# Performance work log

Hardware: AMD Instinct MI355X
Metric: run time of the kernel (lower is better)

Reference implementation:

```python
import jax, jax.numpy as jnp
import numpy as np

B, S, D, H = 2, 2048, 2048, 16
HD = D // H          # head dim 128
R = 64               # qk_rope_head_dim
LR = 64              # kv_low_rank_dim
FF = 2048            # ffn_dim per expert
E = 8                # num routed experts
K = 2                # top_k
ROPE_BASE = 10000.0
LN_EPS = 1e-5


def setup_inputs() -> dict:
    key = jax.random.key(0)
    ks = jax.random.split(key, 20)
    def rn(k, shape, fan_in):
        return jax.random.normal(k, shape, jnp.float32) * (1.0 / np.sqrt(fan_in))
    return {
        "hidden_states": jax.random.normal(ks[0], (B, S, D), jnp.float32),
        "position_ids": jnp.arange(S, dtype=jnp.int32)[None, :],
        # attention projections, stored [in, out]
        "Wq": rn(ks[1], (D, D), D), "Wk": rn(ks[2], (D, D), D), "Wv": rn(ks[3], (D, D), D),
        "Wkc": rn(ks[4], (HD, LR), HD), "Wvc": rn(ks[5], (HD, LR), HD),
        "Wqa": rn(ks[6], (HD, LR), HD), "Wqg": rn(ks[7], (HD, HD), HD),
        "Wov": rn(ks[8], (LR, HD), LR), "Wo": rn(ks[9], (D, D), D),
        "ln1_w": jnp.ones((D,), jnp.float32), "ln1_b": jnp.zeros((D,), jnp.float32),
        "ln2_w": jnp.ones((D,), jnp.float32), "ln2_b": jnp.zeros((D,), jnp.float32),
        # MoE
        "Wg": rn(ks[10], (D, E), D),
        "We1": rn(ks[11], (E, D, FF), D), "We2": rn(ks[12], (E, FF, D), FF), "We3": rn(ks[13], (E, D, FF), D),
        "Ws1": rn(ks[14], (D, FF), D), "Ws2": rn(ks[15], (FF, D), FF), "Ws3": rn(ks[16], (D, FF), D),
    }


def _layernorm(x, w, b):
    mu = jnp.mean(x, -1, keepdims=True)
    var = jnp.mean(jnp.square(x - mu), -1, keepdims=True)
    return (x - mu) * jax.lax.rsqrt(var + LN_EPS) * w + b


def _rotate_half(x):
    h = x.shape[-1] // 2
    return jnp.concatenate([-x[..., h:], x[..., :h]], axis=-1)


def _rope_cos_sin(position_ids, dtype):
    inv_freq = 1.0 / (ROPE_BASE ** (jnp.arange(0, R, 2, dtype=jnp.float32) / R))
    t = jnp.arange(S, dtype=jnp.float32)
    freqs = t[:, None] * inv_freq[None, :]           # [S, R/2]
    emb = jnp.concatenate([freqs, freqs], -1)        # [S, R]
    cos = jnp.cos(emb).astype(dtype)[position_ids][:, :, None, :]  # [1,S,1,R]
    sin = jnp.sin(emb).astype(dtype)[position_ids][:, :, None, :]
    return cos, sin


def reference(hidden_states, position_ids, Wq, Wk, Wv, Wkc, Wvc, Wqa, Wqg, Wov, Wo,
              ln1_w, ln1_b, ln2_w, ln2_b, Wg, We1, We2, We3, Ws1, Ws2, Ws3):
    x = _layernorm(hidden_states, ln1_w, ln1_b)
    # ---- MLA attention ----
    q = (x @ Wq).reshape(B, S, H, HD)
    k = (x @ Wk).reshape(B, S, H, HD)
    v = (x @ Wv).reshape(B, S, H, HD)
    cos, sin = _rope_cos_sin(position_ids, x.dtype)
    qr = q[..., :R] * cos + _rotate_half(q[..., :R]) * sin
    kr = k[..., :R] * cos + _rotate_half(k[..., :R]) * sin
    q = jnp.concatenate([qr, q[..., R:]], -1)
    k = jnp.concatenate([kr, k[..., R:]], -1)
    k_c = k @ Wkc                                   # [B,S,H,LR]
    v_c = v @ Wvc                                   # [B,S,H,LR]
    q_a = q @ Wqa                                   # [B,S,H,LR]
    q_gate = q @ Wqg                                # [B,S,H,HD]
    scores = jnp.einsum('bqhr,bkhr->bhqk', q_a, k_c) / np.sqrt(LR)
    attw = jax.nn.softmax(scores.astype(jnp.float32), axis=-1).astype(q.dtype)
    att_c = jnp.einsum('bhqk,bkhr->bqhr', attw, v_c)  # [B,S,H,LR]
    uplift = att_c @ Wov                              # [B,S,H,HD]
    gated = (jax.nn.silu(q_gate) * uplift).reshape(B, S, D)
    attn_out = gated @ Wo
    h = hidden_states + attn_out
    # ---- MoE with shared expert ----
    xf = _layernorm(h, ln2_w, ln2_b).reshape(-1, D)   # [T, D]
    shared = (jax.nn.silu(xf @ Ws1) * (xf @ Ws3)) @ Ws2
    logits = xf @ Wg                                  # [T, E]
    probs = jax.nn.softmax(logits.astype(jnp.float32), axis=-1)
    topw, topi = jax.lax.top_k(probs, K)
    topw = topw / jnp.sum(topw, -1, keepdims=True)
    T = xf.shape[0]
    combine = jnp.zeros((T, E), xf.dtype).at[jnp.arange(T)[:, None], topi].set(topw.astype(xf.dtype))
    h1 = jnp.einsum('td,edf->etf', xf, We1)
    h3 = jnp.einsum('td,edf->etf', xf, We3)
    eout = jnp.einsum('etf,efd->etd', jax.nn.silu(h1) * h3, We2)
    moe = shared + jnp.einsum('te,etd->td', combine, eout)
    return h + moe.reshape(B, S, D)
```

## Files before the change

### kernel.cpp

```cpp
#include <hip/hip_runtime.h>
#include <math.h>

typedef __bf16 bf16;
typedef __bf16 bf16x8 __attribute__((ext_vector_type(8)));
typedef float f32x4 __attribute__((ext_vector_type(4)));

#define B_ 2
#define S_ 2048
#define D_ 2048
#define H_ 16
#define FF_ 2048
#define E_ 8
#define T_ 4096
#define TH_ 65536
#define CAP_ 4096

#define MFMA_(a, b, c) __builtin_amdgcn_mfma_f32_16x16x32_bf16(a, b, c, 0, 0, 0)

__device__ __forceinline__ int swz(int row, int byteoff) {
  return row * 128 + (byteoff ^ ((row & 7) << 4));
}
__device__ __forceinline__ int swzf(int row, int byteoff) {
  return row * 256 + (byteoff ^ ((row & 7) << 5));
}

__device__ __forceinline__ void split2(float x, bf16& h, bf16& m) {
  h = (bf16)x;
  m = (bf16)(x - (float)h);
}

__device__ __forceinline__ void frag_split(const char* p, int off, bf16x8& r0, bf16x8& r1) {
  f32x4 u = *(const f32x4*)(p + off);
  f32x4 v = *(const f32x4*)(p + off + 16);
#pragma unroll
  for (int j = 0; j < 4; j++) { bf16 a, b; split2(u[j], a, b); r0[j] = a; r1[j] = b; }
#pragma unroll
  for (int j = 0; j < 4; j++) { bf16 a, b; split2(v[j], a, b); r0[4 + j] = a; r1[4 + j] = b; }
}

__device__ __forceinline__ f32x4 dot3(bf16x8 a0, bf16x8 a1,
                                      bf16x8 b0, bf16x8 b1, f32x4 c) {
  c = MFMA_(a0, b0, c);
  c = MFMA_(a0, b1, c);
  c = MFMA_(a1, b0, c);
  return c;
}

__device__ __forceinline__ float blk_sum(float v, float* sbuf, int tid) {
#pragma unroll
  for (int mk = 32; mk; mk >>= 1) v += __shfl_xor(v, mk);
  __syncthreads();
  if ((tid & 63) == 0) sbuf[tid >> 6] = v;
  __syncthreads();
  return sbuf[0] + sbuf[1] + sbuf[2] + sbuf[3];
}

__global__ __launch_bounds__(256) void k_transpose32(const float* __restrict__ src,
                                                     float* __restrict__ dst, int R, int C) {
  __shared__ float tile[32][33];
  int tx = threadIdx.x, ty = threadIdx.y;
  int c0 = blockIdx.x * 32, r0 = blockIdx.y * 32;
#pragma unroll
  for (int j = 0; j < 32; j += 8) tile[ty + j][tx] = src[(size_t)(r0 + ty + j) * C + (c0 + tx)];
  __syncthreads();
#pragma unroll
  for (int j = 0; j < 32; j += 8)
    dst[(size_t)(c0 + ty + j) * R + (r0 + tx)] = tile[tx][ty + j];
}

__global__ __launch_bounds__(256) void k_transpose32b3(const float* __restrict__ s0,
                                                       const float* __restrict__ s1x,
                                                       const float* __restrict__ s2,
                                                       float* __restrict__ dbase) {
  __shared__ float tile[32][33];
  int z = blockIdx.z;
  const float* src = z == 0 ? s0 : (z == 1 ? s1x : s2);
  float* dst = dbase + (size_t)z * 8192;
  int tx = threadIdx.x, ty = threadIdx.y;
  int c0 = blockIdx.x * 32, r0 = blockIdx.y * 32;
#pragma unroll
  for (int j = 0; j < 32; j += 8) tile[ty + j][tx] = src[(size_t)(r0 + ty + j) * 64 + (c0 + tx)];
  __syncthreads();
#pragma unroll
  for (int j = 0; j < 32; j += 8)
    dst[(size_t)(c0 + ty + j) * 128 + (r0 + tx)] = tile[tx][ty + j];
}

__global__ __launch_bounds__(256) void k_transpose_sh3(const float* __restrict__ s0,
                                                       const float* __restrict__ s1x,
                                                       const float* __restrict__ s2,
                                                       bf16* __restrict__ dbase) {
  __shared__ float tile[32][33];
  int z = blockIdx.z;
  const float* src = z == 0 ? s0 : (z == 1 ? s1x : s2);
  bf16* dst = dbase + (size_t)z * 4194304;
  int tx = threadIdx.x, ty = threadIdx.y;
  int c0 = blockIdx.x * 32, r0 = blockIdx.y * 32;
#pragma unroll
  for (int j = 0; j < 32; j += 8) tile[ty + j][tx] = src[(size_t)(r0 + ty + j) * 2048 + (c0 + tx)];
  __syncthreads();
#pragma unroll
  for (int j = 0; j < 32; j += 8)
    dst[(size_t)(c0 + ty + j) * 2048 + (r0 + tx)] = (bf16)tile[tx][ty + j];
}

template <int MODE>
__global__ __launch_bounds__(256) void k_transpose_moe(const float* __restrict__ W1,
                                                       const float* __restrict__ W3,
                                                       bf16* __restrict__ dstB, int eBase) {
  __shared__ float tile[32][33];
  int tx = threadIdx.x, ty = threadIdx.y;
  int z = blockIdx.z;
  const float* src;
  if (MODE == 0) src = ((z & 1) ? W3 : W1) + (size_t)(eBase + (z >> 1)) * 4194304;
  else src = W1 + (size_t)(eBase + z) * 4194304;
  bf16* dst = dstB + (size_t)z * 4194304;
  int c0 = blockIdx.x * 32, r0 = blockIdx.y * 32;
#pragma unroll
  for (int j = 0; j < 32; j += 8) tile[ty + j][tx] = src[(size_t)(r0 + ty + j) * 2048 + (c0 + tx)];
  __syncthreads();
#pragma unroll
  for (int j = 0; j < 32; j += 8)
    dst[(size_t)(c0 + ty + j) * 2048 + (r0 + tx)] = (bf16)tile[tx][ty + j];
}

__global__ __launch_bounds__(256) void k_transpose_split(const float* __restrict__ src,
                                                         bf16* __restrict__ dh, bf16* __restrict__ dl,
                                                         int R, int C) {
  __shared__ float tile[32][33];
  int tx = threadIdx.x, ty = threadIdx.y;
  int c0 = blockIdx.x * 32, r0 = blockIdx.y * 32;
#pragma unroll
  for (int j = 0; j < 32; j += 8) tile[ty + j][tx] = src[(size_t)(r0 + ty + j) * C + (c0 + tx)];
  __syncthreads();
#pragma unroll
  for (int j = 0; j < 32; j += 8) {
    float v = tile[tx][ty + j];
    bf16 h, l;
    split2(v, h, l);
    size_t o = (size_t)(c0 + ty + j) * R + (r0 + tx);
    dh[o] = h;
    dl[o] = l;
  }
}

__global__ __launch_bounds__(256) void k_transpose_split3(const float* __restrict__ s0,
                                                          const float* __restrict__ s1x,
                                                          const float* __restrict__ s2,
                                                          bf16* __restrict__ dbase) {
  __shared__ float tile[32][33];
  int z = blockIdx.z;
  const float* src = z == 0 ? s0 : (z == 1 ? s1x : s2);
  bf16* dh = dbase + (size_t)z * 8388608;
  bf16* dl = dh + 4194304;
  int tx = threadIdx.x, ty = threadIdx.y;
  int c0 = blockIdx.x * 32, r0 = blockIdx.y * 32;
#pragma unroll
  for (int j = 0; j < 32; j += 8) tile[ty + j][tx] = src[(size_t)(r0 + ty + j) * 2048 + (c0 + tx)];
  __syncthreads();
#pragma unroll
  for (int j = 0; j < 32; j += 8) {
    float v = tile[tx][ty + j];
    bf16 h, l;
    split2(v, h, l);
    size_t o = (size_t)(c0 + ty + j) * 2048 + (r0 + tx);
    dh[o] = h;
    dl[o] = l;
  }
}

__global__ __launch_bounds__(256) void k_tr_v32s(const float* __restrict__ vc,
                                                 bf16* __restrict__ vh, bf16* __restrict__ vl) {
  __shared__ float tile[32][33];
  int tx = threadIdx.x, ty = threadIdx.y;
  int z = blockIdx.z;
  int s0 = blockIdx.x * 32, r0 = blockIdx.y * 32;
  int b = z >> 4, h = z & 15;
#pragma unroll
  for (int j = 0; j < 32; j += 8) {
    int s = s0 + ty + j;
    tile[ty + j][tx] = vc[((size_t)((b * S_ + s) * H_ + h)) * 64 + r0 + tx];
  }
  __syncthreads();
#pragma unroll
  for (int j = 0; j < 32; j += 8) {
    int r = r0 + ty + j;
    float v = tile[tx][ty + j];
    bf16 hh, ll;
    split2(v, hh, ll);
    size_t o = ((size_t)(z * 64 + r)) * S_ + s0 + tx;
    vh[o] = hh;
    vl[o] = ll;
  }
}

__global__ __launch_bounds__(256) void k_ln32_split(const float* __restrict__ x, const float* __restrict__ w,
                                                    const float* __restrict__ bb,
                                                    bf16* __restrict__ oh, bf16* __restrict__ ol) {
  __shared__ float sbuf[4];
  int row = blockIdx.x, tid = threadIdx.x;
  const float* xr = x + (size_t)row * D_;
  float v[8];
  float s = 0.f;
#pragma unroll
  for (int j = 0; j < 8; j++) { v[j] = xr[tid + 256 * j]; s += v[j]; }
  float mu = blk_sum(s, sbuf, tid) * (1.f / D_);
  float qs = 0.f;
#pragma unroll
  for (int j = 0; j < 8; j++) { float d = v[j] - mu; qs += d * d; }
  float rs = rsqrtf(blk_sum(qs, sbuf, tid) * (1.f / D_) + 1e-5f);
#pragma unroll
  for (int j = 0; j < 8; j++) {
    int c = tid + 256 * j;
    float xn = (v[j] - mu) * rs * w[c] + bb[c];
    bf16 h, l;
    split2(xn, h, l);
    oh[(size_t)row * D_ + c] = h;
    ol[(size_t)row * D_ + c] = l;
  }
}

template <int EPI>
__global__ __launch_bounds__(256) void k_gemm32s(const bf16* __restrict__ Ah, const bf16* __restrict__ Al, int lda,
                                                 const bf16* __restrict__ Bh, const bf16* __restrict__ Bl, int ldb,
                                                 float* __restrict__ C, int ldc,
                                                 int M, int N, int Kd,
                                                 const float* __restrict__ resid) {
  __shared__ __align__(16) char Ahs[16384];
  __shared__ __align__(16) char Als[16384];
  __shared__ __align__(16) char Bhs[16384];
  __shared__ __align__(16) char Bls[16384];
  int bm = blockIdx.y * 128, bn = blockIdx.x * 128;
  int tid = threadIdx.x;
  int srow = tid >> 3, scol = (tid & 7) * 8;
  int arow[4], brow[4];
#pragma unroll
  for (int i = 0; i < 4; i++) {
    int r = bm + srow + 32 * i;
    arow[i] = r < M ? r : (M - 1);
    int q = bn + srow + 32 * i;
    brow[i] = q < N ? q : (N - 1);
  }
  f32x4 acc[4][4] = {};
  int lane = tid & 63, w = tid >> 6, g = lane >> 4, lr = lane & 15;
  int wm = (w >> 1) * 64, wn = (w & 1) * 64;
  for (int kt = 0; kt < Kd; kt += 64) {
#pragma unroll
    for (int i = 0; i < 4; i++) {
      int o = swz(srow + 32 * i, scol * 2);
      *(uint4*)(Ahs + o) = *(const uint4*)(Ah + (size_t)arow[i] * lda + kt + scol);
      *(uint4*)(Als + o) = *(const uint4*)(Al + (size_t)arow[i] * lda + kt + scol);
      *(uint4*)(Bhs + o) = *(const uint4*)(Bh + (size_t)brow[i] * ldb + kt + scol);
      *(uint4*)(Bls + o) = *(const uint4*)(Bl + (size_t)brow[i] * ldb + kt + scol);
    }
    __syncthreads();
#pragma unroll
    for (int ks = 0; ks < 2; ks++) {
      bf16x8 ah[4], al[4], bh[4], bl[4];
#pragma unroll
      for (int m = 0; m < 4; m++) {
        ah[m] = *(const bf16x8*)(Ahs + swz(wm + m * 16 + lr, ks * 64 + g * 16));
        al[m] = *(const bf16x8*)(Als + swz(wm + m * 16 + lr, ks * 64 + g * 16));
      }
#pragma unroll
      for (int n = 0; n < 4; n++) {
        bh[n] = *(const bf16x8*)(Bhs + swz(wn + n * 16 + lr, ks * 64 + g * 16));
        bl[n] = *(const bf16x8*)(Bls + swz(wn + n * 16 + lr, ks * 64 + g * 16));
      }
#pragma unroll
      for (int m = 0; m < 4; m++)
#pragma unroll
        for (int n = 0; n < 4; n++)
          acc[m][n] = dot3(ah[m], al[m], bh[n], bl[n], acc[m][n]);
    }
    __syncthreads();
  }
#pragma unroll
  for (int m = 0; m < 4; m++)
#pragma unroll
    for (int n = 0; n < 4; n++)
#pragma unroll
      for (int r = 0; r < 4; r++) {
        int row = bm + wm + m * 16 + g * 4 + r;
        int col = bn + wn + n * 16 + lr;
        if (row < M && col < N) {
          float val = acc[m][n][r];
          if (EPI == 1) val += resid[(size_t)row * ldc + col];
          C[(size_t)row * ldc + col] = val;
        }
      }
}

__global__ __launch_bounds__(256) void k_gemm32s_qkv(const bf16* __restrict__ Ah, const bf16* __restrict__ Al,
                                                     const bf16* __restrict__ Bhb,
                                                     float* __restrict__ Cb) {
  int z = blockIdx.z;
  const bf16* Bh = Bhb + (size_t)z * 8388608;
  const bf16* Bl = Bh + 4194304;
  float* C = Cb + (size_t)z * 8388608;
  __shared__ __align__(16) char Ahs[16384];
  __shared__ __align__(16) char Als[16384];
  __shared__ __align__(16) char Bhs[16384];
  __shared__ __align__(16) char Bls[16384];
  int bm = blockIdx.y * 128, bn = blockIdx.x * 128;
  int tid = threadIdx.x;
  int srow = tid >> 3, scol = (tid & 7) * 8;
  f32x4 acc[4][4] = {};
  int lane = tid & 63, w = tid >> 6, g = lane >> 4, lr = lane & 15;
  int wm = (w >> 1) * 64, wn = (w & 1) * 64;
  for (int kt = 0; kt < 2048; kt += 64) {
#pragma unroll
    for (int i = 0; i < 4; i++) {
      int row = srow + 32 * i;
      int o = swz(row, scol * 2);
      *(uint4*)(Ahs + o) = *(const uint4*)(Ah + (size_t)(bm + row) * 2048 + kt + scol);
      *(uint4*)(Als + o) = *(const uint4*)(Al + (size_t)(bm + row) * 2048 + kt + scol);
      *(uint4*)(Bhs + o) = *(const uint4*)(Bh + (size_t)(bn + row) * 2048 + kt + scol);
      *(uint4*)(Bls + o) = *(const uint4*)(Bl + (size_t)(bn + row) * 2048 + kt + scol);
    }
    __syncthreads();
#pragma unroll
    for (int ks = 0; ks < 2; ks++) {
      bf16x8 ah[4], al[4], bh[4], bl[4];
#pragma unroll
      for (int m = 0; m < 4; m++) {
        ah[m] = *(const bf16x8*)(Ahs + swz(wm + m * 16 + lr, ks * 64 + g * 16));
        al[m] = *(const bf16x8*)(Als + swz(wm + m * 16 + lr, ks * 64 + g * 16));
      }
#pragma unroll
      for (int n = 0; n < 4; n++) {
        bh[n] = *(const bf16x8*)(Bhs + swz(wn + n * 16 + lr, ks * 64 + g * 16));
        bl[n] = *(const bf16x8*)(Bls + swz(wn + n * 16 + lr, ks * 64 + g * 16));
      }
#pragma unroll
      for (int m = 0; m < 4; m++)
#pragma unroll
        for (int n = 0; n < 4; n++)
          acc[m][n] = dot3(ah[m], al[m], bh[n], bl[n], acc[m][n]);
    }
    __syncthreads();
  }
#pragma unroll
  for (int m = 0; m < 4; m++)
#pragma unroll
    for (int n = 0; n < 4; n++)
#pragma unroll
      for (int r = 0; r < 4; r++) {
        int row = bm + wm + m * 16 + g * 4 + r;
        int col = bn + wn + n * 16 + lr;
        C[(size_t)row * 2048 + col] = acc[m][n][r];
      }
}

template <int EPI>
__global__ __launch_bounds__(256) void k_gemm32(const float* __restrict__ A, int lda,
                                                const float* __restrict__ Bt, int ldb,
                                                float* __restrict__ C, int ldc,
                                                int M, int N, int Kd,
                                                bf16* __restrict__ Ch, bf16* __restrict__ Cl) {
  __shared__ __align__(16) char As[32768];
  __shared__ __align__(16) char Bs[32768];
  int bm = blockIdx.y * 128, bn = blockIdx.x * 128;
  int tid = threadIdx.x;
  int srow = tid >> 3, scol = (tid & 7) * 8;
  int arow[4], brow[4];
#pragma unroll
  for (int i = 0; i < 4; i++) {
    int r = bm + srow + 32 * i;
    arow[i] = r < M ? r : (M - 1);
    int q = bn + srow + 32 * i;
    brow[i] = q < N ? q : (N - 1);
  }
  f32x4 acc[4][4] = {};
  int lane = tid & 63, w = tid >> 6, g = lane >> 4, lr = lane & 15;
  int wm = (w >> 1) * 64, wn = (w & 1) * 64;
  for (int kt = 0; kt < Kd; kt += 64) {
#pragma unroll
    for (int i = 0; i < 4; i++) {
      const float* pa = A + (size_t)arow[i] * lda + kt + scol;
      f32x4 va0 = *(const f32x4*)pa, va1 = *(const f32x4*)(pa + 4);
      const float* pb = Bt + (size_t)brow[i] * ldb + kt + scol;
      f32x4 vb0 = *(const f32x4*)pb, vb1 = *(const f32x4*)(pb + 4);
      int o = swzf(srow + 32 * i, scol * 4);
      *(f32x4*)(As + o) = va0;
      *(f32x4*)(As + o + 16) = va1;
      *(f32x4*)(Bs + o) = vb0;
      *(f32x4*)(Bs + o + 16) = vb1;
    }
    __syncthreads();
#pragma unroll
    for (int ks = 0; ks < 2; ks++) {
      bf16x8 a0[4], a1[4], b0[4], b1[4];
#pragma unroll
      for (int m = 0; m < 4; m++)
        frag_split(As, swzf(wm + m * 16 + lr, ks * 128 + g * 32), a0[m], a1[m]);
#pragma unroll
      for (int n = 0; n < 4; n++)
        frag_split(Bs, swzf(wn + n * 16 + lr, ks * 128 + g * 32), b0[n], b1[n]);
#pragma unroll
      for (int m = 0; m < 4; m++)
#pragma unroll
        for (int n = 0; n < 4; n++)
          acc[m][n] = dot3(a0[m], a1[m], b0[n], b1[n], acc[m][n]);
    }
    __syncthreads();
  }
#pragma unroll
  for (int m = 0; m < 4; m++)
#pragma unroll
    for (int n = 0; n < 4; n++)
#pragma unroll
      for (int r = 0; r < 4; r++) {
        int row = bm + wm + m * 16 + g * 4 + r;
        int col = bn + wn + n * 16 + lr;
        if (row < M && col < N) {
          C[(size_t)row * ldc + col] = acc[m][n][r];
        }
      }
}

__global__ __launch_bounds__(256) void k_projn64(const float* __restrict__ Ab,
                                                 const float* __restrict__ Btb,
                                                 bf16* __restrict__ Pb,
                                                 float* __restrict__ Vb) {
  int z = blockIdx.z;
  const float* A = Ab + (size_t)z * 8388608;
  const float* Bt = Btb + (size_t)z * 8192;
  __shared__ __align__(16) char As[32768];
  __shared__ __align__(16) char Bs[16384];
  int bm = blockIdx.y * 128;
  int tid = threadIdx.x;
  int lane = tid & 63, w = tid >> 6, g = lane >> 4, lr = lane & 15;
  int arowB = tid >> 2;
  int acol = (tid & 3) * 16;
  f32x4 acc[2][4] = {};
  for (int kt = 0; kt < 128; kt += 64) {
#pragma unroll
    for (int i = 0; i < 2; i++) {
      int row = arowB + 64 * i;
      const float* pa = A + (size_t)(bm + row) * 128 + kt + acol;
#pragma unroll
      for (int j = 0; j < 4; j++)
        *(f32x4*)(As + swzf(row, (acol + j * 4) * 4)) = *(const f32x4*)(pa + j * 4);
    }
    {
      const float* pb = Bt + (size_t)arowB * 128 + kt + acol;
#pragma unroll
      for (int j = 0; j < 4; j++)
        *(f32x4*)(Bs + swzf(arowB, (acol + j * 4) * 4)) = *(const f32x4*)(pb + j * 4);
    }
    __syncthreads();
#pragma unroll
    for (int ks = 0; ks < 2; ks++) {
      bf16x8 a0[2], a1[2], b0[4], b1[4];
#pragma unroll
      for (int m = 0; m < 2; m++)
        frag_split(As, swzf(w * 32 + m * 16 + lr, ks * 128 + g * 32), a0[m], a1[m]);
#pragma unroll
      for (int n = 0; n < 4; n++)
        frag_split(Bs, swzf(n * 16 + lr, ks * 128 + g * 32), b0[n], b1[n]);
#pragma unroll
      for (int m = 0; m < 2; m++)
#pragma unroll
        for (int n = 0; n < 4; n++)
          acc[m][n] = dot3(a0[m], a1[m], b0[n], b1[n], acc[m][n]);
    }
    __syncthreads();
  }
  bf16* Ph = Pb + (size_t)z * 8388608;
  bf16* Pl = Ph + 4194304;
#pragma unroll
  for (int m = 0; m < 2; m++)
#pragma unroll
    for (int n = 0; n < 4; n++)
#pragma unroll
      for (int r = 0; r < 4; r++) {
        int row = bm + w * 32 + m * 16 + g * 4 + r;
        int col = n * 16 + lr;
        size_t o = (size_t)row * 64 + col;
        float val = acc[m][n][r];
        if (z == 2) {
          Vb[o] = val;
        } else {
          bf16 h, l;
          split2(val, h, l);
          Ph[o] = h;
          Pl[o] = l;
        }
      }
}

__global__ __launch_bounds__(256) void k_rope32(float* __restrict__ q, float* __restrict__ k) {
  int idx = blockIdx.x * 256 + threadIdx.x;
  int i = idx & 31, rowth = idx >> 5;
  int s = (rowth >> 4) & (S_ - 1);
  size_t base = (size_t)rowth * 128;
  float freq = expf(-0.28782313662425576f * (float)i);
  float ang = (float)s * freq;
  float sn, cs;
  sincosf(ang, &sn, &cs);
  float q1 = q[base + i], q2 = q[base + i + 32];
  q[base + i] = q1 * cs - q2 * sn;
  q[base + i + 32] = q2 * cs + q1 * sn;
  float k1 = k[base + i], k2 = k[base + i + 32];
  k[base + i] = k1 * cs - k2 * sn;
  k[base + i + 32] = k2 * cs + k1 * sn;
}

__global__ __launch_bounds__(256) void k_attn32p(const bf16* __restrict__ qh, const bf16* __restrict__ ql,
                                                 const bf16* __restrict__ kh, const bf16* __restrict__ kl,
                                                 const bf16* __restrict__ vh, const bf16* __restrict__ vl,
                                                 float* __restrict__ attc) {
  __shared__ __align__(16) char L[65536];
  int qt = blockIdx.x, bh = blockIdx.y;
  int b = bh >> 4, h = bh & 15;
  int tid = threadIdx.x, lane = tid & 63, w = tid >> 6, g = lane >> 4, lr = lane & 15;
  int s0 = qt * 128;
  int srow = tid >> 3, scol = (tid & 7) * 8;
  char* Qsh = L;
  char* Qsl = L + 16384;
#pragma unroll
  for (int i = 0; i < 4; i++) {
    int row = srow + 32 * i;
    size_t goff = ((size_t)((b * S_ + s0 + row) * H_ + h)) * 64 + scol;
    int o = swz(row, scol * 2);
    *(uint4*)(Qsh + o) = *(const uint4*)(qh + goff);
    *(uint4*)(Qsl + o) = *(const uint4*)(ql + goff);
  }
  __syncthreads();
  bf16x8 qf0[2][2], qf1[2][2];
#pragma unroll
  for (int m = 0; m < 2; m++)
#pragma unroll
    for (int ks = 0; ks < 2; ks++) {
      qf0[m][ks] = *(const bf16x8*)(Qsh + swz(w * 32 + m * 16 + lr, ks * 64 + g * 16));
      qf1[m][ks] = *(const bf16x8*)(Qsl + swz(w * 32 + m * 16 + lr, ks * 64 + g * 16));
    }
  __syncthreads();
  char* Ksh = L;
  char* Ksl = L + 8192;
  char* Vsh = L + 16384;
  char* Vsl = L + 24576;
  char* Ph = L + 32768 + w * 8192;
  char* Pl = Ph + 4096;
  f32x4 acc[2][4] = {};
  float mrun[2][4], lrun[2][4];
#pragma unroll
  for (int m = 0; m < 2; m++)
#pragma unroll
    for (int r = 0; r < 4; r++) { mrun[m][r] = -1e30f; lrun[m][r] = 0.f; }
  for (int kt = 0; kt < S_; kt += 64) {
#pragma unroll
    for (int i = 0; i < 2; i++) {
      int rr = srow + 32 * i;
      size_t koff = ((size_t)((b * S_ + kt + rr) * H_ + h)) * 64 + scol;
      size_t voff = ((size_t)(bh * 64 + rr)) * S_ + kt + scol;
      int o = swz(rr, scol * 2);
      *(uint4*)(Ksh + o) = *(const uint4*)(kh + koff);
      *(uint4*)(Ksl + o) = *(const uint4*)(kl + koff);
      *(uint4*)(Vsh + o) = *(const uint4*)(vh + voff);
      *(uint4*)(Vsl + o) = *(const uint4*)(vl + voff);
    }
    __syncthreads();
    f32x4 sc[2][4] = {};
#pragma unroll
    for (int ks = 0; ks < 2; ks++) {
      bf16x8 k0[4], k1[4];
#pragma unroll
      for (int n = 0; n < 4; n++) {
        k0[n] = *(const bf16x8*)(Ksh + swz(n * 16 + lr, ks * 64 + g * 16));
        k1[n] = *(const bf16x8*)(Ksl + swz(n * 16 + lr, ks * 64 + g * 16));
      }
      __builtin_amdgcn_s_setprio(1);
#pragma unroll
      for (int m = 0; m < 2; m++)
#pragma unroll
        for (int n = 0; n < 4; n++)
          sc[m][n] = dot3(qf0[m][ks], qf1[m][ks], k0[n], k1[n], sc[m][n]);
      __builtin_amdgcn_s_setprio(0);
    }
#pragma unroll
    for (int m = 0; m < 2; m++)
#pragma unroll
      for (int r = 0; r < 4; r++) {
        float a0 = sc[m][0][r] * 0.125f, a1 = sc[m][1][r] * 0.125f;
        float a2 = sc[m][2][r] * 0.125f, a3 = sc[m][3][r] * 0.125f;
        float mx = fmaxf(fmaxf(a0, a1), fmaxf(a2, a3));
#pragma unroll
        for (int mk = 1; mk < 16; mk <<= 1) mx = fmaxf(mx, __shfl_xor(mx, mk));
        float mo = mrun[m][r];
        float mn = fmaxf(mo, mx);
        float f = expf(mo - mn);
        float p0 = expf(a0 - mn), p1 = expf(a1 - mn), p2 = expf(a2 - mn), p3 = expf(a3 - mn);
        int prow = m * 16 + g * 4 + r;
        bf16 h0, l0, h1, l1, h2, l2, h3, l3;
        split2(p0, h0, l0);
        split2(p1, h1, l1);
        split2(p2, h2, l2);
        split2(p3, h3, l3);
        *(bf16*)(Ph + swz(prow, lr * 2)) = h0;
        *(bf16*)(Pl + swz(prow, lr * 2)) = l0;
        *(bf16*)(Ph + swz(prow, 32 + lr * 2)) = h1;
        *(bf16*)(Pl + swz(prow, 32 + lr * 2)) = l1;
        *(bf16*)(Ph + swz(prow, 64 + lr * 2)) = h2;
        *(bf16*)(Pl + swz(prow, 64 + lr * 2)) = l2;
        *(bf16*)(Ph + swz(prow, 96 + lr * 2)) = h3;
        *(bf16*)(Pl + swz(prow, 96 + lr * 2)) = l3;
        float ps = p0 + p1 + p2 + p3;
#pragma unroll
        for (int mk = 1; mk < 16; mk <<= 1) ps += __shfl_xor(ps, mk);
        lrun[m][r] = lrun[m][r] * f + ps;
        mrun[m][r] = mn;
#pragma unroll
        for (int n = 0; n < 4; n++) acc[m][n][r] *= f;
      }
#pragma unroll
    for (int ks = 0; ks < 2; ks++) {
      bf16x8 p0f[2], p1f[2], v0f[4], v1f[4];
#pragma unroll
      for (int m = 0; m < 2; m++) {
        p0f[m] = *(const bf16x8*)(Ph + swz(m * 16 + lr, ks * 64 + g * 16));
        p1f[m] = *(const bf16x8*)(Pl + swz(m * 16 + lr, ks * 64 + g * 16));
      }
#pragma unroll
      for (int n = 0; n < 4; n++) {
        v0f[n] = *(const bf16x8*)(Vsh + swz(n * 16 + lr, ks * 64 + g * 16));
        v1f[n] = *(const bf16x8*)(Vsl + swz(n * 16 + lr, ks * 64 + g * 16));
      }
      __builtin_amdgcn_s_setprio(1);
#pragma unroll
      for (int m = 0; m < 2; m++)
#pragma unroll
        for (int n = 0; n < 4; n++)
          acc[m][n] = dot3(p0f[m], p1f[m], v0f[n], v1f[n], acc[m][n]);
      __builtin_amdgcn_s_setprio(0);
    }
    __syncthreads();
  }
#pragma unroll
  for (int m = 0; m < 2; m++)
#pragma unroll
    for (int n = 0; n < 4; n++)
#pragma unroll
      for (int r = 0; r < 4; r++) {
        int s = s0 + w * 32 + m * 16 + g * 4 + r;
        attc[((size_t)((b * S_ + s) * H_ + h)) * 64 + n * 16 + lr] = acc[m][n][r] / lrun[m][r];
      }
}

__global__ __launch_bounds__(256) void k_silu32_split(const float* __restrict__ a, const float* __restrict__ b,
                                                      bf16* __restrict__ ch, bf16* __restrict__ cl, long n) {
  long i = ((long)blockIdx.x * 256 + threadIdx.x) * 8;
  if (i >= n) return;
  f32x4 av0 = *(const f32x4*)(a + i), av1 = *(const f32x4*)(a + i + 4);
  f32x4 bv0 = *(const f32x4*)(b + i), bv1 = *(const f32x4*)(b + i + 4);
  bf16x8 hv, lv;
#pragma unroll
  for (int j = 0; j < 4; j++) {
    float x = av0[j];
    float g = x / (1.f + expf(-x)) * bv0[j];
    bf16 h, l;
    split2(g, h, l);
    hv[j] = h; lv[j] = l;
  }
#pragma unroll
  for (int j = 0; j < 4; j++) {
    float x = av1[j];
    float g = x / (1.f + expf(-x)) * bv1[j];
    bf16 h, l;
    split2(g, h, l);
    hv[4 + j] = h; lv[4 + j] = l;
  }
  *(bf16x8*)(ch + i) = hv;
  *(bf16x8*)(cl + i) = lv;
}

__global__ __launch_bounds__(256) void k_router(const float* __restrict__ hbuf,
                                                const float* __restrict__ w2, const float* __restrict__ b2,
                                                const float* __restrict__ Wg, bf16* __restrict__ xf,
                                                int* __restrict__ count, int* __restrict__ permg,
                                                int* __restrict__ permt, float* __restrict__ wslot) {
  __shared__ float sbuf[4];
  int t = blockIdx.x, tid = threadIdx.x;
  const float* hr = hbuf + (size_t)t * D_;
  float v[8];
  float s = 0.f;
#pragma unroll
  for (int j = 0; j < 8; j++) { v[j] = hr[tid + 256 * j]; s += v[j]; }
  float mu = blk_sum(s, sbuf, tid) * (1.f / D_);
  float qs = 0.f;
#pragma unroll
  for (int j = 0; j < 8; j++) { float d = v[j] - mu; qs += d * d; }
  float rs = rsqrtf(blk_sum(qs, sbuf, tid) * (1.f / D_) + 1e-5f);
  float le[8] = {0, 0, 0, 0, 0, 0, 0, 0};
#pragma unroll
  for (int j = 0; j < 8; j++) {
    int c = tid + 256 * j;
    float xn = (v[j] - mu) * rs * w2[c] + b2[c];
    xf[(size_t)t * D_ + c] = (bf16)xn;
    const float* wr = Wg + (size_t)c * 8;
#pragma unroll
    for (int e = 0; e < 8; e++) le[e] += xn * wr[e];
  }
#pragma unroll
  for (int e = 0; e < 8; e++) le[e] = blk_sum(le[e], sbuf, tid);
  if (tid == 0) {
    float mx = le[0];
    for (int e = 1; e < 8; e++) mx = fmaxf(mx, le[e]);
    float p[8], sum = 0.f;
    for (int e = 0; e < 8; e++) { p[e] = expf(le[e] - mx); sum += p[e]; }
    int i0 = 0;
    for (int e = 1; e < 8; e++) if (p[e] > p[i0]) i0 = e;
    int i1 = (i0 == 0) ? 1 : 0;
    for (int e = 0; e < 8; e++) if (e != i0 && p[e] > p[i1]) i1 = e;
    float inv = 1.f / (p[i0] + p[i1]);
    int pos0 = atomicAdd(&count[i0], 1);
    permg[i0 * CAP_ + pos0] = 2 * t;
    permt[i0 * CAP_ + pos0] = t;
    int pos1 = atomicAdd(&count[i1], 1);
    permg[i1 * CAP_ + pos1] = 2 * t + 1;
    permt[i1 * CAP_ + pos1] = t;
    wslot[2 * t] = p[i0] * inv;
    wslot[2 * t + 1] = p[i1] * inv;
  }
}

template <bool GATHER>
__global__ __launch_bounds__(256) void k_gemm(const bf16* __restrict__ A, int lda,
                                              const bf16* __restrict__ Bt, int ldb,
                                              bf16* __restrict__ C, int ldc, int M, int N, int Kd,
                                              const int* __restrict__ amap,
                                              const int* __restrict__ cmap,
                                              const int* __restrict__ countp) {
  int Mz = countp ? countp[0] : M;
  int bm = blockIdx.y * 128, bn = blockIdx.x * 128;
  if (bm >= Mz) return;
  __shared__ __align__(16) char As[16384];
  __shared__ __align__(16) char Bs[16384];
  int tid = threadIdx.x;
  int srow = tid >> 3, scol = (tid & 7) * 8;
  int arow[4], brow[4];
#pragma unroll
  for (int i = 0; i < 4; i++) {
    int r = bm + srow + 32 * i;
    if (GATHER) { int rc = r < Mz ? r : (Mz - 1); arow[i] = amap[rc]; }
    else { arow[i] = r < M ? r : (M - 1); }
    int bq = bn + srow + 32 * i;
    brow[i] = bq < N ? bq : (N - 1);
  }
  f32x4 acc[4][4] = {};
  int lane = tid & 63, w = tid >> 6, g = lane >> 4, lr = lane & 15;
  int wm = (w >> 1) * 64, wn = (w & 1) * 64;
  for (int kt = 0; kt < Kd; kt += 64) {
#pragma unroll
    for (int i = 0; i < 4; i++) {
      uint4 da = *(const uint4*)(A + (size_t)arow[i] * lda + kt + scol);
      *(uint4*)(As + swz(srow + 32 * i, scol * 2)) = da;
      uint4 db = *(const uint4*)(Bt + (size_t)brow[i] * ldb + kt + scol);
      *(uint4*)(Bs + swz(srow + 32 * i, scol * 2)) = db;
    }
    __syncthreads();
#pragma unroll
    for (int ks = 0; ks < 2; ks++) {
      bf16x8 af[4], bfr[4];
#pragma unroll
      for (int m = 0; m < 4; m++) af[m] = *(const bf16x8*)(As + swz(wm + m * 16 + lr, ks * 64 + g * 16));
#pragma unroll
      for (int n = 0; n < 4; n++) bfr[n] = *(const bf16x8*)(Bs + swz(wn + n * 16 + lr, ks * 64 + g * 16));
#pragma unroll
      for (int m = 0; m < 4; m++)
#pragma unroll
        for (int n = 0; n < 4; n++)
          acc[m][n] = MFMA_(af[m], bfr[n], acc[m][n]);
    }
    __syncthreads();
  }
#pragma unroll
  for (int m = 0; m < 4; m++)
#pragma unroll
    for (int n = 0; n < 4; n++)
#pragma unroll
      for (int r = 0; r < 4; r++) {
        int row = bm + wm + m * 16 + g * 4 + r;
        int col = bn + wn + n * 16 + lr;
        if (row < Mz && col < N) {
          size_t orow = cmap ? (size_t)cmap[row] : (size_t)row;
          C[orow * ldc + col] = (bf16)acc[m][n][r];
        }
      }
}

template <int MODE>
__global__ __launch_bounds__(256) void k_gemm_moe(const bf16* __restrict__ A, int lda,
                                                  const bf16* __restrict__ wteB,
                                                  bf16* __restrict__ C0, bf16* __restrict__ C1, int ldc,
                                                  int N, int Kd,
                                                  const int* __restrict__ permt, const int* __restrict__ permg,
                                                  const int* __restrict__ count, int eBase) {
  int z = blockIdx.z;
  int e;
  const int* amap;
  const int* cmap;
  bf16* C;
  if (MODE == 0) {
    e = eBase + (z >> 1);
    amap = permt + e * CAP_;
    cmap = permg + e * CAP_;
    C = (z & 1) ? C1 : C0;
  } else {
    e = eBase + z;
    amap = permg + e * CAP_;
    cmap = permg + e * CAP_;
    C = C0;
  }
  const bf16* Bt = wteB + (size_t)z * 4194304;
  int Mz = count[e];
  int bm = blockIdx.y * 128, bn = blockIdx.x * 128;
  if (bm >= Mz) return;
  __shared__ __align__(16) char As[16384];
  __shared__ __align__(16) char Bs[16384];
  int tid = threadIdx.x;
  int srow = tid >> 3, scol = (tid & 7) * 8;
  int arow[4], brow[4];
#pragma unroll
  for (int i = 0; i < 4; i++) {
    int r = bm + srow + 32 * i;
    int rc = r < Mz ? r : (Mz - 1);
    arow[i] = amap[rc];
    int bq = bn + srow + 32 * i;
    brow[i] = bq < N ? bq : (N - 1);
  }
  f32x4 acc[4][4] = {};
  int lane = tid & 63, w = tid >> 6, g = lane >> 4, lr = lane & 15;
  int wm = (w >> 1) * 64, wn = (w & 1) * 64;
  for (int kt = 0; kt < Kd; kt += 64) {
#pragma unroll
    for (int i = 0; i < 4; i++) {
      uint4 da = *(const uint4*)(A + (size_t)arow[i] * lda + kt + scol);
      *(uint4*)(As + swz(srow + 32 * i, scol * 2)) = da;
      uint4 db = *(const uint4*)(Bt + (size_t)brow[i] * 2048 + kt + scol);
      *(uint4*)(Bs + swz(srow + 32 * i, scol * 2)) = db;
    }
    __syncthreads();
#pragma unroll
    for (int ks = 0; ks < 2; ks++) {
      bf16x8 af[4], bfr[4];
#pragma unroll
      for (int m = 0; m < 4; m++) af[m] = *(const bf16x8*)(As + swz(wm + m * 16 + lr, ks * 64 + g * 16));
#pragma unroll
      for (int n = 0; n < 4; n++) bfr[n] = *(const bf16x8*)(Bs + swz(wn + n * 16 + lr, ks * 64 + g * 16));
#pragma unroll
      for (int m = 0; m < 4; m++)
#pragma unroll
        for (int n = 0; n < 4; n++)
          acc[m][n] = MFMA_(af[m], bfr[n], acc[m][n]);
    }
    __syncthreads();
  }
#pragma unroll
  for (int m = 0; m < 4; m++)
#pragma unroll
    for (int n = 0; n < 4; n++)
#pragma unroll
      for (int r = 0; r < 4; r++) {
        int row = bm + wm + m * 16 + g * 4 + r;
        int col = bn + wn + n * 16 + lr;
        if (row < Mz && col < N) {
          C[(size_t)cmap[row] * ldc + col] = (bf16)acc[m][n][r];
        }
      }
}

__global__ __launch_bounds__(256) void k_silu_mul(const bf16* __restrict__ a, const bf16* __restrict__ b,
                                                  bf16* __restrict__ c, long n) {
  long i = ((long)blockIdx.x * 256 + threadIdx.x) * 8;
  if (i >= n) return;
  bf16x8 av = *(const bf16x8*)(a + i);
  bf16x8 bv = *(const bf16x8*)(b + i);
  bf16x8 cv;
#pragma unroll
  for (int j = 0; j < 8; j++) {
    float x = (float)av[j];
    float y = (float)bv[j];
    cv[j] = (bf16)(x / (1.f + expf(-x)) * y);
  }
  *(bf16x8*)(c + i) = cv;
}

__global__ __launch_bounds__(256) void k_combine(const float* __restrict__ hbuf, const bf16* __restrict__ shr,
                                                 const bf16* __restrict__ eout, const float* __restrict__ wslot,
                                                 float* __restrict__ out) {
  long i = ((long)blockIdx.x * 256 + threadIdx.x) * 4;
  int t = (int)(i >> 11);
  int c = (int)(i & (D_ - 1));
  float w0 = wslot[2 * t], w1 = wslot[2 * t + 1];
  float4 hv = *(const float4*)(hbuf + i);
  const bf16* s4 = shr + i;
  const bf16* e0 = eout + ((size_t)(2 * t)) * D_ + c;
  const bf16* e1 = e0 + D_;
  float4 o;
  o.x = hv.x + (float)s4[0] + w0 * (float)e0[0] + w1 * (float)e1[0];
  o.y = hv.y + (float)s4[1] + w0 * (float)e0[1] + w1 * (float)e1[1];
  o.z = hv.z + (float)s4[2] + w0 * (float)e0[2] + w1 * (float)e1[2];
  o.w = hv.w + (float)s4[3] + w0 * (float)e0[3] + w1 * (float)e1[3];
  *(float4*)(out + i) = o;
}

extern "C" void kernel_launch(void* const* d_in, const int* in_sizes, int n_in, void* d_out,
                              int out_size, void* d_ws, size_t ws_size, hipStream_t stream) {
  const float* hidden = (const float*)d_in[0];
  const float* Wq = (const float*)d_in[2];
  const float* Wk = (const float*)d_in[3];
  const float* Wv = (const float*)d_in[4];
  const float* Wkc = (const float*)d_in[5];
  const float* Wvc = (const float*)d_in[6];
  const float* Wqa = (const float*)d_in[7];
  const float* Wqg = (const float*)d_in[8];
  const float* Wov = (const float*)d_in[9];
  const float* Wo = (const float*)d_in[10];
  const float* ln1w = (const float*)d_in[11];
  const float* ln1b = (const float*)d_in[12];
  const float* ln2w = (const float*)d_in[13];
  const float* ln2b = (const float*)d_in[14];
  const float* Wg = (const float*)d_in[15];
  const float* We1 = (const float*)d_in[16];
  const float* We2 = (const float*)d_in[17];
  const float* We3 = (const float*)d_in[18];
  const float* Ws1 = (const float*)d_in[19];
  const float* Ws2 = (const float*)d_in[20];
  const float* Ws3 = (const float*)d_in[21];
  float* out = (float*)d_out;
  (void)in_sizes; (void)n_in; (void)out_size;

  const size_t MB = 1ull << 20;
  char* base = (char*)d_ws;
  float* hbuf = (float*)(base);
  bf16* shr = (bf16*)(base + 32 * MB);
  int* count = (int*)(base + 48 * MB);
  int* permg = (int*)(base + 48 * MB + 4096);
  int* permt = (int*)(base + 48 * MB + 4096 + 131072);
  float* wslot = (float*)(base + 48 * MB + 4096 + 262144);
  float* wtqa32 = (float*)(base + 49 * MB);
  float* wtov32 = (float*)(base + 49 * MB + 98304);
  float* wtqg32 = (float*)(base + 49 * MB + 131072);
  char* A0p = base + 50 * MB;
  char* A1p = base + 82 * MB;
  char* A2p = base + 114 * MB;
  char* A3p = base + 146 * MB;
  char* A4p = base + 178 * MB;
  char* A5p = base + 210 * MB;
  if (ws_size < 242 * MB) return;

  bf16* xln_h = (bf16*)A0p;
  bf16* xln_l = (bf16*)(A0p + 16 * MB);
  bf16* wtqkv = (bf16*)A1p;
  float* qb = (float*)A3p;
  float* kb = (float*)A4p;
  float* vb = (float*)A5p;
  bf16* qab_h = (bf16*)A1p;
  bf16* qab_l = (bf16*)(A1p + 8 * MB);
  bf16* kcb_h = (bf16*)(A1p + 16 * MB);
  bf16* kcb_l = (bf16*)(A1p + 24 * MB);
  float* vcb = (float*)A2p;
  bf16* vct_h = (bf16*)(A2p + 16 * MB);
  bf16* vct_l = (bf16*)(A2p + 24 * MB);
  float* qgate = (float*)A0p;
  float* attc = (float*)A3p;
  bf16* wto_h = (bf16*)(A3p + 16 * MB);
  bf16* wto_l = (bf16*)(A3p + 24 * MB);
  float* uplift = (float*)A4p;
  bf16* gated_h = (bf16*)A5p;
  bf16* gated_l = (bf16*)(A5p + 16 * MB);
  bf16* xf = (bf16*)A1p;
  bf16* s1 = (bf16*)(A1p + 16 * MB);
  bf16* wts1 = (bf16*)A2p;
  bf16* wts3 = (bf16*)(A2p + 8 * MB);
  bf16* wts2 = (bf16*)(A2p + 16 * MB);
  bf16* s3 = (bf16*)A3p;
  bf16* wteB_mid = (bf16*)A2p;
  bf16* wteB_out = (bf16*)A1p;
  bf16* mid1 = (bf16*)A4p;
  bf16* mid3 = (bf16*)A5p;
  bf16* midg = (bf16*)A0p;
  bf16* eout = (bf16*)A3p;

  hipMemsetAsync(count, 0, 256, stream);

  dim3 tb(32, 8);
  k_transpose_split3<<<dim3(64, 64, 3), tb, 0, stream>>>(Wq, Wk, Wv, wtqkv);
  k_transpose32b3<<<dim3(2, 4, 3), tb, 0, stream>>>(Wqa, Wkc, Wvc, wtqa32);
  k_transpose32<<<dim3(4, 4, 1), tb, 0, stream>>>(Wqg, wtqg32, 128, 128);
  k_transpose32<<<dim3(4, 2, 1), tb, 0, stream>>>(Wov, wtov32, 64, 128);

  k_ln32_split<<<T_, 256, 0, stream>>>(hidden, ln1w, ln1b, xln_h, xln_l);

  k_gemm32s_qkv<<<dim3(16, 32, 3), 256, 0, stream>>>(xln_h, xln_l, wtqkv, qb);

  k_rope32<<<8192, 256, 0, stream>>>(qb, kb);

  k_projn64<<<dim3(1, 512, 3), 256, 0, stream>>>(qb, wtqa32, qab_h, vcb);
  k_gemm32<0><<<dim3(1, 512, 1), 256, 0, stream>>>(qb, 128, wtqg32, 128, qgate, 128, TH_, 128, 128, nullptr, nullptr);

  k_tr_v32s<<<dim3(64, 2, 32), tb, 0, stream>>>(vcb, vct_h, vct_l);
  k_transpose_split<<<dim3(64, 64, 1), tb, 0, stream>>>(Wo, wto_h, wto_l, 2048, 2048);

  k_attn32p<<<dim3(16, 32, 1), 256, 0, stream>>>(qab_h, qab_l, kcb_h, kcb_l, vct_h, vct_l, attc);

  k_transpose_sh3<<<dim3(64, 64, 3), tb, 0, stream>>>(Ws1, Ws3, Ws2, wts1);

  k_gemm32<0><<<dim3(1, 512, 1), 256, 0, stream>>>(attc, 64, wtov32, 64, uplift, 128, TH_, 128, 64, nullptr, nullptr);
  k_silu32_split<<<4096, 256, 0, stream>>>(qgate, uplift, gated_h, gated_l, (long)TH_ * 128);
  k_gemm32s<1><<<dim3(16, 32, 1), 256, 0, stream>>>(gated_h, gated_l, 2048, wto_h, wto_l, 2048, hbuf, 2048, T_, 2048, 2048, hidden);

  k_router<<<T_, 256, 0, stream>>>(hbuf, ln2w, ln2b, Wg, xf, count, permg, permt, wslot);

  k_gemm<false><<<dim3(16, 32, 1), 256, 0, stream>>>(xf, 2048, wts1, 2048, s1, 2048, T_, 2048, 2048, nullptr, nullptr, nullptr);
  k_gemm<false><<<dim3(16, 32, 1), 256, 0, stream>>>(xf, 2048, wts3, 2048, s3, 2048, T_, 2048, 2048, nullptr, nullptr, nullptr);
  k_silu_mul<<<4096, 256, 0, stream>>>(s1, s3, s1, (long)T_ * 2048);
  k_gemm<false><<<dim3(16, 32, 1), 256, 0, stream>>>(s1, 2048, wts2, 2048, shr, 2048, T_, 2048, 2048, nullptr, nullptr, nullptr);

  for (int p = 0; p < 2; p++) {
    k_transpose_moe<0><<<dim3(64, 64, 8), tb, 0, stream>>>(We1, We3, wteB_mid, 4 * p);
    k_gemm_moe<0><<<dim3(16, 32, 8), 256, 0, stream>>>(xf, 2048, wteB_mid, mid1, mid3, 2048, 2048, 2048, permt, permg, count, 4 * p);
  }
  k_silu_mul<<<8192, 256, 0, stream>>>(mid1, mid3, midg, (long)2 * T_ * 2048);
  k_transpose_moe<1><<<dim3(64, 64, 8), tb, 0, stream>>>(We2, nullptr, wteB_out, 0);
  k_gemm_moe<1><<<dim3(16, 32, 8), 256, 0, stream>>>(midg, 2048, wteB_out, eout, nullptr, 2048, 2048, 2048, permt, permg, count, 0);

  k_combine<<<8192, 256, 0, stream>>>(hbuf, shr, eout, wslot, out);
}
```

Baseline: 1.608 ms.

## Fuse fp32 weight transpose-convert into MoE and shared-expert GEMM loads

```diff
diff --git a/kernel.cpp b/kernel.cpp
--- a/kernel.cpp
+++ b/kernel.cpp
@@ -2,6 +2,7 @@
 #include <math.h>
 
 typedef __bf16 bf16;
+typedef __bf16 bf16x4 __attribute__((ext_vector_type(4)));
 typedef __bf16 bf16x8 __attribute__((ext_vector_type(8)));
 typedef float f32x4 __attribute__((ext_vector_type(4)));
 
@@ -84,44 +85,6 @@
 #pragma unroll
   for (int j = 0; j < 32; j += 8)
     dst[(size_t)(c0 + ty + j) * 128 + (r0 + tx)] = tile[tx][ty + j];
-}
-
-__global__ __launch_bounds__(256) void k_transpose_sh3(const float* __restrict__ s0,
-                                                       const float* __restrict__ s1x,
-                                                       const float* __restrict__ s2,
-                                                       bf16* __restrict__ dbase) {
-  __shared__ float tile[32][33];
-  int z = blockIdx.z;
-  const float* src = z == 0 ? s0 : (z == 1 ? s1x : s2);
-  bf16* dst = dbase + (size_t)z * 4194304;
-  int tx = threadIdx.x, ty = threadIdx.y;
-  int c0 = blockIdx.x * 32, r0 = blockIdx.y * 32;
-#pragma unroll
-  for (int j = 0; j < 32; j += 8) tile[ty + j][tx] = src[(size_t)(r0 + ty + j) * 2048 + (c0 + tx)];
-  __syncthreads();
-#pragma unroll
-  for (int j = 0; j < 32; j += 8)
-    dst[(size_t)(c0 + ty + j) * 2048 + (r0 + tx)] = (bf16)tile[tx][ty + j];
-}
-
-template <int MODE>
-__global__ __launch_bounds__(256) void k_transpose_moe(const float* __restrict__ W1,
-                                                       const float* __restrict__ W3,
-                                                       bf16* __restrict__ dstB, int eBase) {
-  __shared__ float tile[32][33];
-  int tx = threadIdx.x, ty = threadIdx.y;
-  int z = blockIdx.z;
-  const float* src;
-  if (MODE == 0) src = ((z & 1) ? W3 : W1) + (size_t)(eBase + (z >> 1)) * 4194304;
-  else src = W1 + (size_t)(eBase + z) * 4194304;
-  bf16* dst = dstB + (size_t)z * 4194304;
-  int c0 = blockIdx.x * 32, r0 = blockIdx.y * 32;
-#pragma unroll
-  for (int j = 0; j < 32; j += 8) tile[ty + j][tx] = src[(size_t)(r0 + ty + j) * 2048 + (c0 + tx)];
-  __syncthreads();
-#pragma unroll
-  for (int j = 0; j < 32; j += 8)
-    dst[(size_t)(c0 + ty + j) * 2048 + (r0 + tx)] = (bf16)tile[tx][ty + j];
 }
 
 __global__ __launch_bounds__(256) void k_transpose_split(const float* __restrict__ src,
@@ -725,39 +688,102 @@
   }
 }
 
-template <bool GATHER>
-__global__ __launch_bounds__(256) void k_gemm(const bf16* __restrict__ A, int lda,
-                                              const bf16* __restrict__ Bt, int ldb,
-                                              bf16* __restrict__ C, int ldc, int M, int N, int Kd,
-                                              const int* __restrict__ amap,
-                                              const int* __restrict__ cmap,
-                                              const int* __restrict__ countp) {
-  int Mz = countp ? countp[0] : M;
+template <int MODE>
+__global__ __launch_bounds__(256) void k_gemm_nt(
+    const bf16* __restrict__ Amoe, const bf16* __restrict__ Ash,
+    const float* __restrict__ W1, const float* __restrict__ W3,
+    const float* __restrict__ Wsa, const float* __restrict__ Wsb,
+    bf16* __restrict__ C0, bf16* __restrict__ C1,
+    bf16* __restrict__ Cs0, bf16* __restrict__ Cs1,
+    const int* __restrict__ permt, const int* __restrict__ permg,
+    const int* __restrict__ count) {
+  int z = blockIdx.z;
+  const bf16* A;
+  const float* Bsrc;
+  bf16* C;
+  const int* amap = nullptr;
+  const int* cmap = nullptr;
+  int Mz;
+  if (MODE == 0) {
+    if (z < 16) {
+      int e = z >> 1;
+      Bsrc = ((z & 1) ? W3 : W1) + (size_t)e * 4194304;
+      A = Amoe;
+      C = (z & 1) ? C1 : C0;
+      amap = permt + e * CAP_;
+      cmap = permg + e * CAP_;
+      Mz = count[e];
+    } else {
+      Bsrc = (z == 16) ? Wsa : Wsb;
+      A = Ash;
+      C = (z == 16) ? Cs0 : Cs1;
+      Mz = T_;
+    }
+  } else {
+    if (z < 8) {
+      Bsrc = W1 + (size_t)z * 4194304;
+      A = Amoe;
+      C = C0;
+      amap = permg + z * CAP_;
+      cmap = permg + z * CAP_;
+      Mz = count[z];
+    } else {
+      Bsrc = Wsa;
+      A = Ash;
+      C = Cs0;
+      Mz = T_;
+    }
+  }
   int bm = blockIdx.y * 128, bn = blockIdx.x * 128;
   if (bm >= Mz) return;
   __shared__ __align__(16) char As[16384];
   __shared__ __align__(16) char Bs[16384];
   int tid = threadIdx.x;
   int srow = tid >> 3, scol = (tid & 7) * 8;
-  int arow[4], brow[4];
+  int arow[4];
 #pragma unroll
   for (int i = 0; i < 4; i++) {
     int r = bm + srow + 32 * i;
-    if (GATHER) { int rc = r < Mz ? r : (Mz - 1); arow[i] = amap[rc]; }
-    else { arow[i] = r < M ? r : (M - 1); }
-    int bq = bn + srow + 32 * i;
-    brow[i] = bq < N ? bq : (N - 1);
-  }
+    int rc = r < Mz ? r : (Mz - 1);
+    arow[i] = amap ? amap[rc] : rc;
+  }
+  int nseg = (tid & 15) * 8;
+  int kb = (tid >> 4) * 4;
   f32x4 acc[4][4] = {};
   int lane = tid & 63, w = tid >> 6, g = lane >> 4, lr = lane & 15;
   int wm = (w >> 1) * 64, wn = (w & 1) * 64;
-  for (int kt = 0; kt < Kd; kt += 64) {
+  for (int kt = 0; kt < 2048; kt += 64) {
 #pragma unroll
     for (int i = 0; i < 4; i++) {
-      uint4 da = *(const uint4*)(A + (size_t)arow[i] * lda + kt + scol);
+      uint4 da = *(const uint4*)(A + (size_t)arow[i] * 2048 + kt + scol);
       *(uint4*)(As + swz(srow + 32 * i, scol * 2)) = da;
-      uint4 db = *(const uint4*)(Bt + (size_t)brow[i] * ldb + kt + scol);
-      *(uint4*)(Bs + swz(srow + 32 * i, scol * 2)) = db;
+    }
+    {
+      const float* pb = Bsrc + (size_t)(kt + kb) * 2048 + bn + nseg;
+      f32x4 b0a = *(const f32x4*)pb, b0b = *(const f32x4*)(pb + 4);
+      f32x4 b1a = *(const f32x4*)(pb + 2048), b1b = *(const f32x4*)(pb + 2052);
+      f32x4 b2a = *(const f32x4*)(pb + 4096), b2b = *(const f32x4*)(pb + 4100);
+      f32x4 b3a = *(const f32x4*)(pb + 6144), b3b = *(const f32x4*)(pb + 6148);
+#pragma unroll
+      for (int j = 0; j < 4; j++) {
+        int n = nseg + j;
+        bf16x4 pk;
+        pk[0] = (bf16)b0a[j];
+        pk[1] = (bf16)b1a[j];
+        pk[2] = (bf16)b2a[j];
+        pk[3] = (bf16)b3a[j];
+        *(bf16x4*)(Bs + (n * 128 + ((kb * 2) ^ ((n & 7) << 4)))) = pk;
+      }
+#pragma unroll
+      for (int j = 0; j < 4; j++) {
+        int n = nseg + 4 + j;
+        bf16x4 pk;
+        pk[0] = (bf16)b0b[j];
+        pk[1] = (bf16)b1b[j];
+        pk[2] = (bf16)b2b[j];
+        pk[3] = (bf16)b3b[j];
+        *(bf16x4*)(Bs + (n * 128 + ((kb * 2) ^ ((n & 7) << 4)))) = pk;
+      }
     }
     __syncthreads();
 #pragma unroll
@@ -783,90 +809,9 @@
       for (int r = 0; r < 4; r++) {
         int row = bm + wm + m * 16 + g * 4 + r;
         int col = bn + wn + n * 16 + lr;
-        if (row < Mz && col < N) {
+        if (row < Mz) {
           size_t orow = cmap ? (size_t)cmap[row] : (size_t)row;
-          C[orow * ldc + col] = (bf16)acc[m][n][r];
-        }
-      }
-}
-
-template <int MODE>
-__global__ __launch_bounds__(256) void k_gemm_moe(const bf16* __restrict__ A, int lda,
-                                                  const bf16* __restrict__ wteB,
-                                                  bf16* __restrict__ C0, bf16* __restrict__ C1, int ldc,
-                                                  int N, int Kd,
-                                                  const int* __restrict__ permt, const int* __restrict__ permg,
-                                                  const int* __restrict__ count, int eBase) {
-  int z = blockIdx.z;
-  int e;
-  const int* amap;
-  const int* cmap;
-  bf16* C;
-  if (MODE == 0) {
-    e = eBase + (z >> 1);
-    amap = permt + e * CAP_;
-    cmap = permg + e * CAP_;
-    C = (z & 1) ? C1 : C0;
-  } else {
-    e = eBase + z;
-    amap = permg + e * CAP_;
-    cmap = permg + e * CAP_;
-    C = C0;
-  }
-  const bf16* Bt = wteB + (size_t)z * 4194304;
-  int Mz = count[e];
-  int bm = blockIdx.y * 128, bn = blockIdx.x * 128;
-  if (bm >= Mz) return;
-  __shared__ __align__(16) char As[16384];
-  __shared__ __align__(16) char Bs[16384];
-  int tid = threadIdx.x;
-  int srow = tid >> 3, scol = (tid & 7) * 8;
-  int arow[4], brow[4];
-#pragma unroll
-  for (int i = 0; i < 4; i++) {
-    int r = bm + srow + 32 * i;
-    int rc = r < Mz ? r : (Mz - 1);
-    arow[i] = amap[rc];
-    int bq = bn + srow + 32 * i;
-    brow[i] = bq < N ? bq : (N - 1);
-  }
-  f32x4 acc[4][4] = {};
-  int lane = tid & 63, w = tid >> 6, g = lane >> 4, lr = lane & 15;
-  int wm = (w >> 1) * 64, wn = (w & 1) * 64;
-  for (int kt = 0; kt < Kd; kt += 64) {
-#pragma unroll
-    for (int i = 0; i < 4; i++) {
-      uint4 da = *(const uint4*)(A + (size_t)arow[i] * lda + kt + scol);
-      *(uint4*)(As + swz(srow + 32 * i, scol * 2)) = da;
-      uint4 db = *(const uint4*)(Bt + (size_t)brow[i] * 2048 + kt + scol);
-      *(uint4*)(Bs + swz(srow + 32 * i, scol * 2)) = db;
-    }
-    __syncthreads();
-#pragma unroll
-    for (int ks = 0; ks < 2; ks++) {
-      bf16x8 af[4], bfr[4];
-#pragma unroll
-      for (int m = 0; m < 4; m++) af[m] = *(const bf16x8*)(As + swz(wm + m * 16 + lr, ks * 64 + g * 16));
-#pragma unroll
-      for (int n = 0; n < 4; n++) bfr[n] = *(const bf16x8*)(Bs + swz(wn + n * 16 + lr, ks * 64 + g * 16));
-#pragma unroll
-      for (int m = 0; m < 4; m++)
-#pragma unroll
-        for (int n = 0; n < 4; n++)
-          acc[m][n] = MFMA_(af[m], bfr[n], acc[m][n]);
-    }
-    __syncthreads();
-  }
-#pragma unroll
-  for (int m = 0; m < 4; m++)
-#pragma unroll
-    for (int n = 0; n < 4; n++)
-#pragma unroll
-      for (int r = 0; r < 4; r++) {
-        int row = bm + wm + m * 16 + g * 4 + r;
-        int col = bn + wn + n * 16 + lr;
-        if (row < Mz && col < N) {
-          C[(size_t)cmap[row] * ldc + col] = (bf16)acc[m][n][r];
+          C[orow * 2048 + col] = (bf16)acc[m][n][r];
         }
       }
 }
@@ -973,12 +918,7 @@
   bf16* gated_l = (bf16*)(A5p + 16 * MB);
   bf16* xf = (bf16*)A1p;
   bf16* s1 = (bf16*)(A1p + 16 * MB);
-  bf16* wts1 = (bf16*)A2p;
-  bf16* wts3 = (bf16*)(A2p + 8 * MB);
-  bf16* wts2 = (bf16*)(A2p + 16 * MB);
   bf16* s3 = (bf16*)A3p;
-  bf16* wteB_mid = (bf16*)A2p;
-  bf16* wteB_out = (bf16*)A1p;
   bf16* mid1 = (bf16*)A4p;
   bf16* mid3 = (bf16*)A5p;
   bf16* midg = (bf16*)A0p;
@@ -1006,26 +946,18 @@
 
   k_attn32p<<<dim3(16, 32, 1), 256, 0, stream>>>(qab_h, qab_l, kcb_h, kcb_l, vct_h, vct_l, attc);
 
-  k_transpose_sh3<<<dim3(64, 64, 3), tb, 0, stream>>>(Ws1, Ws3, Ws2, wts1);
-
   k_gemm32<0><<<dim3(1, 512, 1), 256, 0, stream>>>(attc, 64, wtov32, 64, uplift, 128, TH_, 128, 64, nullptr, nullptr);
   k_silu32_split<<<4096, 256, 0, stream>>>(qgate, uplift, gated_h, gated_l, (long)TH_ * 128);
   k_gemm32s<1><<<dim3(16, 32, 1), 256, 0, stream>>>(gated_h, gated_l, 2048, wto_h, wto_l, 2048, hbuf, 2048, T_, 2048, 2048, hidden);
 
   k_router<<<T_, 256, 0, stream>>>(hbuf, ln2w, ln2b, Wg, xf, count, permg, permt, wslot);
 
-  k_gemm<false><<<dim3(16, 32, 1), 256, 0, stream>>>(xf, 2048, wts1, 2048, s1, 2048, T_, 2048, 2048, nullptr, nullptr, nullptr);
-  k_gemm<false><<<dim3(16, 32, 1), 256, 0, stream>>>(xf, 2048, wts3, 2048, s3, 2048, T_, 2048, 2048, nullptr, nullptr, nullptr);
+  k_gemm_nt<0><<<dim3(16, 32, 18), 256, 0, stream>>>(xf, xf, We1, We3, Ws1, Ws3,
+                                                     mid1, mid3, s1, s3, permt, permg, count);
   k_silu_mul<<<4096, 256, 0, stream>>>(s1, s3, s1, (long)T_ * 2048);
-  k_gemm<false><<<dim3(16, 32, 1), 256, 0, stream>>>(s1, 2048, wts2, 2048, shr, 2048, T_, 2048, 2048, nullptr, nullptr, nullptr);
-
-  for (int p = 0; p < 2; p++) {
-    k_transpose_moe<0><<<dim3(64, 64, 8), tb, 0, stream>>>(We1, We3, wteB_mid, 4 * p);
-    k_gemm_moe<0><<<dim3(16, 32, 8), 256, 0, stream>>>(xf, 2048, wteB_mid, mid1, mid3, 2048, 2048, 2048, permt, permg, count, 4 * p);
-  }
   k_silu_mul<<<8192, 256, 0, stream>>>(mid1, mid3, midg, (long)2 * T_ * 2048);
-  k_transpose_moe<1><<<dim3(64, 64, 8), tb, 0, stream>>>(We2, nullptr, wteB_out, 0);
-  k_gemm_moe<1><<<dim3(16, 32, 8), 256, 0, stream>>>(midg, 2048, wteB_out, eout, nullptr, 2048, 2048, 2048, permt, permg, count, 0);
+  k_gemm_nt<1><<<dim3(16, 32, 9), 256, 0, stream>>>(midg, s1, We2, nullptr, Ws2, nullptr,
+                                                    eout, nullptr, shr, nullptr, permt, permg, count);
 
   k_combine<<<8192, 256, 0, stream>>>(hbuf, shr, eout, wslot, out);
 }
```

Result: slower. 2.000 ms (+24.4%).
